# Performance work log

Hardware: AMD Instinct MI355X
Metric: run time of the kernel (lower is better)

The kernel has to match this reference:

```python
import jax, jax.numpy as jnp
import numpy as np

B = 32          # batch_size
S = 64          # num_subgraph
D = 8           # dim_multi_hot (module-level global in source repo)
NE = S * D      # num_edges = 512
NNODES = 1024
E = 150000      # incidence rows
IN_UNITS = [16, 32, 32]
OUT_UNITS = [32, 32, 16]


def _glorot(key, shape):
    # glorot_normal over last two dims (out, in)
    fan_out, fan_in = shape[-2], shape[-1]
    std = (2.0 / (fan_in + fan_out)) ** 0.5
    return std * jax.random.normal(key, shape, dtype=jnp.float32)


def setup_inputs() -> dict:
    key = jax.random.key(0)
    ks = jax.random.split(key, 10)
    nodes_features = jax.random.normal(ks[0], (NNODES * S, IN_UNITS[0]), dtype=jnp.float32)
    c0 = jax.random.randint(ks[1], (E,), 0, B, dtype=jnp.int32)
    c1 = jax.random.randint(ks[2], (E,), 0, NNODES, dtype=jnp.int32)
    c2 = jax.random.randint(ks[3], (E,), 0, S, dtype=jnp.int32)
    c3 = jax.random.randint(ks[4], (E,), 0, D, dtype=jnp.int32)
    incidence_matrix = jnp.stack([c0, c1, c2, c3], axis=1)
    return {
        'nodes_features': nodes_features,
        'in_core0': _glorot(ks[5], (NE, IN_UNITS[1], IN_UNITS[0])),
        'in_bias0': jnp.zeros((NE, IN_UNITS[1], 1), jnp.float32),
        'in_core1': _glorot(ks[6], (NE, IN_UNITS[2], IN_UNITS[1])),
        'in_bias1': jnp.zeros((NE, IN_UNITS[2], 1), jnp.float32),
        'out_core0': _glorot(ks[7], (NE, OUT_UNITS[1], OUT_UNITS[0])),
        'out_bias0': jnp.zeros((NE, OUT_UNITS[1], 1), jnp.float32),
        'out_core1': _glorot(ks[8], (NE, OUT_UNITS[2], OUT_UNITS[1])),
        'out_bias1': jnp.zeros((NE, OUT_UNITS[2], 1), jnp.float32),
        'incidence_matrix': incidence_matrix,
    }


def reference(nodes_features, in_core0, in_bias0, in_core1, in_bias1,
              out_core0, out_bias0, out_core1, out_bias1, incidence_matrix):
    c0 = incidence_matrix[:, 0]
    c1 = incidence_matrix[:, 1]
    c2 = incidence_matrix[:, 2]
    c3 = incidence_matrix[:, 3]

    # gather node features per incidence row: [E, in0]
    x = nodes_features[c1 * S + c2]
    eidx = c2 * D + c3  # per-edge weight index, < NE

    # per-edge MLP (gathered batched matmul + bias + relu)
    for W, b in ((in_core0, in_bias0), (in_core1, in_bias1)):
        x = jax.nn.relu(jnp.einsum('eoi,ei->eo', W[eidx], x) + b[eidx, :, 0])

    # unsorted segment mean over irregular edge groups
    seg = c0 * (D * S) + c2 * D + c3
    nseg = B * S * D
    sums = jax.ops.segment_sum(x, seg, num_segments=nseg)           # [B*NE, 32]
    cnt = jax.ops.segment_sum(jnp.ones((x.shape[0], 1), x.dtype), seg, num_segments=nseg)
    ef = jnp.where(cnt > 0, sums / jnp.maximum(cnt, 1.0), 0.0)       # [B*NE, 32]

    # output MLP: weights tiled over batch (einsum avoids explicit repeat)
    ef = ef.reshape(B, NE, -1)
    for W, b in ((out_core0, out_bias0), (out_core1, out_bias1)):
        ef = jax.nn.relu(jnp.einsum('eoi,bei->beo', W, ef) + b[None, :, :, 0])

    return ef.reshape(B * NE, OUT_UNITS[-1], 1)
```

## Files before the change

### kernel.cpp

```cpp
#include <hip/hip_runtime.h>

#define B_    32
#define S_    64
#define D_    8
#define NE_   512
#define E_    150000
#define CAP   448

#define SC_BLK   1024
#define SC_EPT   4
#define SC_EPB   (SC_BLK * SC_EPT)
#define SC_GRID  ((E_ + SC_EPB - 1) / SC_EPB)
#define SLOTS    32
#define PITCH    (SC_GRID * SLOTS)

#define PAYLOAD_BYTE_OFF 131072

typedef __attribute__((ext_vector_type(8)))  short  short8;
typedef __attribute__((ext_vector_type(16))) float  float16;

__device__ __forceinline__ unsigned short f2bf(float f) {
    union { float f; unsigned int u; } cv; cv.f = f;
    unsigned int u = cv.u;
    return (unsigned short)((u + 0x7fffu + ((u >> 16) & 1u)) >> 16);
}
__device__ __forceinline__ unsigned int pack2bf(float a, float b) {
    return (unsigned int)f2bf(a) | ((unsigned int)f2bf(b) << 16);
}

__global__ __launch_bounds__(SC_BLK)
void scatter_bin(const int* __restrict__ inc,
                 int* __restrict__ cnt2D,
                 int* __restrict__ payload2D) {
    __shared__ int lcount[NE_];
    const int tid = threadIdx.x;

    if (tid < NE_) lcount[tid] = 0;
    __syncthreads();

    int ei[SC_EPT], lp[SC_EPT], pl[SC_EPT];
    #pragma unroll
    for (int i = 0; i < SC_EPT; ++i) {
        const int e = blockIdx.x * SC_EPB + i * SC_BLK + tid;
        ei[i] = -1;
        if (e < E_) {
            const int4 c = ((const int4*)inc)[e];
            ei[i] = c.z * D_ + c.w;
            pl[i] = (c.x << 16) | (c.y * S_ + c.z);
            lp[i] = atomicAdd(&lcount[ei[i]], 1);
        }
    }
    #pragma unroll
    for (int i = 0; i < SC_EPT; ++i)
        if (ei[i] >= 0 && lp[i] < SLOTS)
            payload2D[ei[i] * PITCH + blockIdx.x * SLOTS + lp[i]] = pl[i];
    __syncthreads();
    if (tid < NE_)
        cnt2D[tid * SC_GRID + blockIdx.x] = min(lcount[tid], SLOTS);
}


#define TILE_COMPUTE(bXv, pvv, vldv)                                            \
  {                                                                             \
    float16 c0;                                                                 \
    _Pragma("unroll")                                                           \
    for (int r = 0; r < 16; ++r)                                                \
        c0[r] = bias0s[(r & 3) + 8 * (r >> 2) + 4 * q];                         \
    c0 = __builtin_amdgcn_mfma_f32_32x32x16_bf16(aWa, (bXv), c0, 0, 0, 0);      \
    unsigned Pw[8];                                                             \
    _Pragma("unroll")                                                           \
    for (int j = 0; j < 8; ++j)                                                 \
        Pw[j] = pack2bf(fmaxf(c0[2 * j], 0.f), fmaxf(c0[2 * j + 1], 0.f));      \
    asm("v_permlane32_swap_b32 %0, %1" : "+v"(Pw[0]), "+v"(Pw[2]));             \
    asm("v_permlane32_swap_b32 %0, %1" : "+v"(Pw[1]), "+v"(Pw[3]));             \
    asm("v_permlane32_swap_b32 %0, %1" : "+v"(Pw[4]), "+v"(Pw[6]));             \
    asm("v_permlane32_swap_b32 %0, %1" : "+v"(Pw[5]), "+v"(Pw[7]));             \
    union { unsigned u[4]; short8 s; } H0c, H1c;                                \
    H0c.u[0] = Pw[0]; H0c.u[1] = Pw[1]; H0c.u[2] = Pw[2]; H0c.u[3] = Pw[3];     \
    H1c.u[0] = Pw[4]; H1c.u[1] = Pw[5]; H1c.u[2] = Pw[6]; H1c.u[3] = Pw[7];     \
    float16 c1;                                                                 \
    _Pragma("unroll")                                                           \
    for (int r = 0; r < 16; ++r)                                                \
        c1[r] = bias1s[(r & 3) + 8 * (r >> 2) + 4 * q];                         \
    c1 = __builtin_amdgcn_mfma_f32_32x32x16_bf16(aWb0, H0c.s, c1, 0, 0, 0);     \
    c1 = __builtin_amdgcn_mfma_f32_32x32x16_bf16(aWb1, H1c.s, c1, 0, 0, 0);     \
    if (vldv) {                                                                 \
        const int b_e = ((pvv) >> 16) & 31;                                     \
        _Pragma("unroll")                                                       \
        for (int r = 0; r < 16; ++r)                                            \
            atomicAdd(&acc[b_e][(r & 3) + 8 * (r >> 2) + 4 * q],                \
                      fmaxf(c1[r], 0.f));                                       \
        if (q == 0) atomicAdd(&cnts[b_e], 1.f);                                 \
    }                                                                           \
  }

__global__ __launch_bounds__(512, 4)
void main_mfma(const float* __restrict__ nf,
               const float* __restrict__ iw0, const float* __restrict__ ib0,
               const float* __restrict__ iw1, const float* __restrict__ ib1,
               const float* __restrict__ ow0, const float* __restrict__ ob0,
               const float* __restrict__ ow1, const float* __restrict__ ob1,
               const int* __restrict__ cnt2D, const int* __restrict__ payload2D,
               float* __restrict__ out) {
    const int bid  = blockIdx.x;
    const int tid  = threadIdx.x;
    const int wav  = tid >> 6;
    const int lane = tid & 63;
    const int e32  = lane & 31;
    const int q    = lane >> 5;

    __shared__ float acc[32][33];
    __shared__ float hb[32][33];
    __shared__ float cnts[32];
    __shared__ float q0t[32 * 33];
    __shared__ float q1t[32 * 17];
    __shared__ float qb0s[32], qb1s[16];
    __shared__ float bias0s[32], bias1s[32];
    __shared__ int   sbase[64], scount[64];
    __shared__ int   sn;
    __shared__ int   elist[512];

    const int* Pb = payload2D + (size_t)bid * PITCH;
    const int p0 = tid, p1 = tid + 512, p2 = tid + 1024;
    const int r0 = Pb[p0];
    const int r1 = Pb[p1];
    const int r2 = (p2 < PITCH) ? Pb[p2] : 0;

    if (tid < 64) {
        int v = (tid < SC_GRID) ? cnt2D[bid * SC_GRID + tid] : 0;
        scount[tid] = v;
        int incl = v;
        #pragma unroll
        for (int off = 1; off < 64; off <<= 1) {
            const int t = __shfl_up(incl, off);
            if (tid >= off) incl += t;
        }
        sbase[tid] = incl - v;
        if (tid == SC_GRID - 1) sn = min(incl, CAP);
    }

    short8 aWa, aWb0, aWb1;
    {
        const float* wa = iw0 + (size_t)bid * 512 + e32 * 16 + q * 8;
        float4 u0 = ((const float4*)wa)[0], u1 = ((const float4*)wa)[1];
        unsigned int p[4] = { pack2bf(u0.x,u0.y), pack2bf(u0.z,u0.w),
                              pack2bf(u1.x,u1.y), pack2bf(u1.z,u1.w) };
        aWa = *(short8*)p;
    }
    {
        const float* wb = iw1 + (size_t)bid * 1024 + e32 * 32 + q * 8;
        float4 u0 = ((const float4*)wb)[0], u1 = ((const float4*)wb)[1];
        unsigned int p[4] = { pack2bf(u0.x,u0.y), pack2bf(u0.z,u0.w),
                              pack2bf(u1.x,u1.y), pack2bf(u1.z,u1.w) };
        aWb0 = *(short8*)p;
        const float* wb2 = wb + 16;
        float4 u2 = ((const float4*)wb2)[0], u3 = ((const float4*)wb2)[1];
        unsigned int p2k[4] = { pack2bf(u2.x,u2.y), pack2bf(u2.z,u2.w),
                                pack2bf(u3.x,u3.y), pack2bf(u3.z,u3.w) };
        aWb1 = *(short8*)p2k;
    }

    for (int i = tid; i < 1024; i += 512) {
        const int o = i >> 5, k = i & 31;
        q0t[k * 33 + o] = ow0[(size_t)bid * 1024 + i];
    }
    { const int o = tid >> 5, k = tid & 31;
      q1t[k * 17 + o] = ow1[(size_t)bid * 512 + tid]; }
    if (tid < 32)       { bias0s[tid] = ib0[bid * 32 + tid]; cnts[tid] = 0.f; }
    else if (tid < 64)  bias1s[tid - 32] = ib1[bid * 32 + (tid - 32)];
    else if (tid < 96)  qb0s[tid - 64] = ob0[bid * 32 + (tid - 64)];
    else if (tid < 112) qb1s[tid - 96] = ob1[bid * 16 + (tid - 96)];
    for (int i = tid; i < 32 * 33; i += 512) ((float*)acc)[i] = 0.f;
    __syncthreads();

    {
        const int blk0 = p0 >> 5, sl0 = p0 & 31;
        if (sl0 < scount[blk0]) {
            const int idx = sbase[blk0] + sl0;
            if (idx < CAP) elist[idx] = r0;
        }
        const int blk1 = p1 >> 5, sl1 = p1 & 31;
        if (sl1 < scount[blk1]) {
            const int idx = sbase[blk1] + sl1;
            if (idx < CAP) elist[idx] = r1;
        }
        if (p2 < PITCH) {
            const int blk2 = p2 >> 5, sl2 = p2 & 31;
            if (sl2 < scount[blk2]) {
                const int idx = sbase[blk2] + sl2;
                if (idx < CAP) elist[idx] = r2;
            }
        }
    }
    __syncthreads();

    const int n  = sn;
    const int s0 = (wav << 5) + e32;
    const int s1 = s0 + 256;
    const int pv0 = elist[s0];
    const int pv1 = elist[s1];
    const bool v0 = s0 < n;
    const bool v1 = s1 < n;

    short8 bX0, bX1;
    {
        const float4* xp = (const float4*)(nf + (size_t)(pv0 & 0xFFFF) * 16 + q * 8);
        float4 u0 = xp[0], u1 = xp[1];
        unsigned int pk[4] = { pack2bf(u0.x,u0.y), pack2bf(u0.z,u0.w),
                               pack2bf(u1.x,u1.y), pack2bf(u1.z,u1.w) };
        bX0 = *(short8*)pk;
    }
    {
        const float4* xp = (const float4*)(nf + (size_t)(pv1 & 0xFFFF) * 16 + q * 8);
        float4 u0 = xp[0], u1 = xp[1];
        unsigned int pk[4] = { pack2bf(u0.x,u0.y), pack2bf(u0.z,u0.w),
                               pack2bf(u1.x,u1.y), pack2bf(u1.z,u1.w) };
        bX1 = *(short8*)pk;
    }

    TILE_COMPUTE(bX0, pv0, v0);
    TILE_COMPUTE(bX1, pv1, v1);
    __syncthreads();

    {
        const int b  = tid >> 4;
        const int j  = tid & 15;
        const float cv  = cnts[b];
        const float inv = cv > 0.f ? 1.0f / cv : 0.0f;
        #pragma unroll
        for (int s = 0; s < 2; ++s) {
            const int oo = j * 2 + s;
            float d = 0.f;
            #pragma unroll
            for (int k = 0; k < 32; ++k) d = fmaf(q0t[k * 33 + oo], acc[b][k], d);
            hb[b][oo] = fmaxf(fmaf(d, inv, qb0s[oo]), 0.f);
        }
    }
    __syncthreads();

    {
        const int b = tid >> 4;
        const int o = tid & 15;
        float d = qb1s[o];
        #pragma unroll
        for (int k = 0; k < 32; ++k) d = fmaf(q1t[k * 17 + o], hb[b][k], d);
        out[((size_t)b * NE_ + bid) * 16 + o] = fmaxf(d, 0.f);
    }
}

extern "C" void kernel_launch(void* const* d_in, const int* in_sizes, int n_in,
                              void* d_out, int out_size, void* d_ws, size_t ws_size,
                              hipStream_t stream) {
    const float* nf  = (const float*)d_in[0];
    const float* iw0 = (const float*)d_in[1];
    const float* ib0 = (const float*)d_in[2];
    const float* iw1 = (const float*)d_in[3];
    const float* ib1 = (const float*)d_in[4];
    const float* ow0 = (const float*)d_in[5];
    const float* ob0 = (const float*)d_in[6];
    const float* ow1 = (const float*)d_in[7];
    const float* ob1 = (const float*)d_in[8];
    const int*   inc = (const int*)d_in[9];

    int* cnt2D     = (int*)d_ws;
    int* payload2D = (int*)((char*)d_ws + PAYLOAD_BYTE_OFF);

    scatter_bin<<<SC_GRID, SC_BLK, 0, stream>>>(inc, cnt2D, payload2D);
    main_mfma<<<NE_, 512, 0, stream>>>(nf, iw0, ib0, iw1, ib1, ow0, ob0, ow1, ob1,
                                       cnt2D, payload2D, (float*)d_out);
}
```

Before: 119.0 us.

## Gather node features before compaction and drop shared-memory scan barriers

Each wave now does the per-block prefix scan itself with shuffles, so the shared scount/sbase arrays and one __syncthreads are gone. Node-feature rows are gathered and packed to bf16 right after the payload load. They are stored into LDS next to the compacted edge list, which removes the dependent global gather after compaction and overlaps it with the weight loads. The two output-MLP stages are merged without a barrier between them, which relies on each batch row's hb being produced within the same wavefront. The trade-off is gathering for every payload slot, including unused ones, plus 16 KB more LDS per block, which may reduce occupancy.

```diff
diff --git a/kernel.cpp b/kernel.cpp
--- a/kernel.cpp
+++ b/kernel.cpp
@@ -94,6 +94,16 @@
     }                                                                           \
   }
 
+#define GATHER_PACK(rowv, LO, HI)                                               \
+  {                                                                             \
+    const float4* xp = (const float4*)(nf + (size_t)(rowv) * 16);               \
+    float4 a0 = xp[0], a1 = xp[1], a2 = xp[2], a3 = xp[3];                      \
+    LO.x = pack2bf(a0.x, a0.y); LO.y = pack2bf(a0.z, a0.w);                     \
+    LO.z = pack2bf(a1.x, a1.y); LO.w = pack2bf(a1.z, a1.w);                     \
+    HI.x = pack2bf(a2.x, a2.y); HI.y = pack2bf(a2.z, a2.w);                     \
+    HI.z = pack2bf(a3.x, a3.y); HI.w = pack2bf(a3.z, a3.w);                     \
+  }
+
 __global__ __launch_bounds__(512, 4)
 void main_mfma(const float* __restrict__ nf,
                const float* __restrict__ iw0, const float* __restrict__ ib0,
@@ -109,6 +119,9 @@
     const int e32  = lane & 31;
     const int q    = lane >> 5;
 
+    __shared__ uint4 xls0[512];
+    __shared__ uint4 xls1[512];
+    __shared__ int   elist[512];
     __shared__ float acc[32][33];
     __shared__ float hb[32][33];
     __shared__ float cnts[32];
@@ -116,28 +129,25 @@
     __shared__ float q1t[32 * 17];
     __shared__ float qb0s[32], qb1s[16];
     __shared__ float bias0s[32], bias1s[32];
-    __shared__ int   sbase[64], scount[64];
-    __shared__ int   sn;
-    __shared__ int   elist[512];
+
 
     const int* Pb = payload2D + (size_t)bid * PITCH;
     const int p0 = tid, p1 = tid + 512, p2 = tid + 1024;
     const int r0 = Pb[p0];
     const int r1 = Pb[p1];
-    const int r2 = (p2 < PITCH) ? Pb[p2] : 0;
-
-    if (tid < 64) {
-        int v = (tid < SC_GRID) ? cnt2D[bid * SC_GRID + tid] : 0;
-        scount[tid] = v;
-        int incl = v;
-        #pragma unroll
-        for (int off = 1; off < 64; off <<= 1) {
-            const int t = __shfl_up(incl, off);
-            if (tid >= off) incl += t;
-        }
-        sbase[tid] = incl - v;
-        if (tid == SC_GRID - 1) sn = min(incl, CAP);
-    }
+    int r2 = 0;
+    if (p2 < PITCH) r2 = Pb[p2];
+
+    int v = 0;
+    if (lane < SC_GRID) v = cnt2D[bid * SC_GRID + lane];
+    int incl = v;
+    #pragma unroll
+    for (int off = 1; off < 64; off <<= 1) {
+        const int t = __shfl_up(incl, off);
+        if (lane >= off) incl += t;
+    }
+    const int excl = incl - v;
+    const int n = min(__shfl(incl, SC_GRID - 1), CAP);
 
     short8 aWa, aWb0, aWb1;
     {
@@ -160,6 +170,11 @@
         aWb1 = *(short8*)p2k;
     }
 
+    uint4 g0lo = {}, g0hi = {}, g1lo = {}, g1hi = {}, g2lo = {}, g2hi = {};
+    GATHER_PACK(r0 & 0xFFFF, g0lo, g0hi);
+    GATHER_PACK(r1 & 0xFFFF, g1lo, g1hi);
+    GATHER_PACK(r2 & 0xFFFF, g2lo, g2hi);
+
     for (int i = tid; i < 1024; i += 512) {
         const int o = i >> 5, k = i & 31;
         q0t[k * 33 + o] = ow0[(size_t)bid * 1024 + i];
@@ -171,52 +186,37 @@
     else if (tid < 96)  qb0s[tid - 64] = ob0[bid * 32 + (tid - 64)];
     else if (tid < 112) qb1s[tid - 96] = ob1[bid * 16 + (tid - 96)];
     for (int i = tid; i < 32 * 33; i += 512) ((float*)acc)[i] = 0.f;
-    __syncthreads();
-
-    {
-        const int blk0 = p0 >> 5, sl0 = p0 & 31;
-        if (sl0 < scount[blk0]) {
-            const int idx = sbase[blk0] + sl0;
-            if (idx < CAP) elist[idx] = r0;
-        }
-        const int blk1 = p1 >> 5, sl1 = p1 & 31;
-        if (sl1 < scount[blk1]) {
-            const int idx = sbase[blk1] + sl1;
-            if (idx < CAP) elist[idx] = r1;
-        }
-        if (p2 < PITCH) {
-            const int blk2 = p2 >> 5, sl2 = p2 & 31;
-            if (sl2 < scount[blk2]) {
-                const int idx = sbase[blk2] + sl2;
-                if (idx < CAP) elist[idx] = r2;
-            }
-        }
-    }
-    __syncthreads();
-
-    const int n  = sn;
+
+    {
+        const int blk0 = p0 >> 5,                 sl0 = p0 & 31;
+        const int blk1 = p1 >> 5,                 sl1 = p1 & 31;
+        const int blk2 = min(p2 >> 5, SC_GRID-1), sl2 = p2 & 31;
+        const int c0_ = __shfl(v, blk0),   b0_ = __shfl(excl, blk0);
+        const int c1_ = __shfl(v, blk1),   b1_ = __shfl(excl, blk1);
+        const int c2_ = __shfl(v, blk2),   b2_ = __shfl(excl, blk2);
+        if (sl0 < c0_) {
+            const int idx = b0_ + sl0;
+            if (idx < CAP) { elist[idx] = r0; xls0[idx] = g0lo; xls1[idx] = g0hi; }
+        }
+        if (sl1 < c1_) {
+            const int idx = b1_ + sl1;
+            if (idx < CAP) { elist[idx] = r1; xls0[idx] = g1lo; xls1[idx] = g1hi; }
+        }
+        if (p2 < PITCH && sl2 < c2_) {
+            const int idx = b2_ + sl2;
+            if (idx < CAP) { elist[idx] = r2; xls0[idx] = g2lo; xls1[idx] = g2hi; }
+        }
+    }
+    __syncthreads();
+
     const int s0 = (wav << 5) + e32;
     const int s1 = s0 + 256;
     const int pv0 = elist[s0];
     const int pv1 = elist[s1];
     const bool v0 = s0 < n;
     const bool v1 = s1 < n;
-
-    short8 bX0, bX1;
-    {
-        const float4* xp = (const float4*)(nf + (size_t)(pv0 & 0xFFFF) * 16 + q * 8);
-        float4 u0 = xp[0], u1 = xp[1];
-        unsigned int pk[4] = { pack2bf(u0.x,u0.y), pack2bf(u0.z,u0.w),
-                               pack2bf(u1.x,u1.y), pack2bf(u1.z,u1.w) };
-        bX0 = *(short8*)pk;
-    }
-    {
-        const float4* xp = (const float4*)(nf + (size_t)(pv1 & 0xFFFF) * 16 + q * 8);
-        float4 u0 = xp[0], u1 = xp[1];
-        unsigned int pk[4] = { pack2bf(u0.x,u0.y), pack2bf(u0.z,u0.w),
-                               pack2bf(u1.x,u1.y), pack2bf(u1.z,u1.w) };
-        bX1 = *(short8*)pk;
-    }
+    const short8 bX0 = *(const short8*)(q ? &xls1[s0] : &xls0[s0]);
+    const short8 bX1 = *(const short8*)(q ? &xls1[s1] : &xls0[s1]);
 
     TILE_COMPUTE(bX0, pv0, v0);
     TILE_COMPUTE(bX1, pv1, v1);
@@ -235,16 +235,10 @@
             for (int k = 0; k < 32; ++k) d = fmaf(q0t[k * 33 + oo], acc[b][k], d);
             hb[b][oo] = fmaxf(fmaf(d, inv, qb0s[oo]), 0.f);
         }
-    }
-    __syncthreads();
-
-    {
-        const int b = tid >> 4;
-        const int o = tid & 15;
-        float d = qb1s[o];
+        float d1 = qb1s[j];
         #pragma unroll
-        for (int k = 0; k < 32; ++k) d = fmaf(q1t[k * 17 + o], hb[b][k], d);
-        out[((size_t)b * NE_ + bid) * 16 + o] = fmaxf(d, 0.f);
+        for (int k = 0; k < 32; ++k) d1 = fmaf(q1t[k * 17 + j], hb[b][k], d1);
+        out[((size_t)b * NE_ + bid) * 16 + j] = fmaxf(d1, 0.f);
     }
 }
 
```

New measurement: 119.5 us. Within noise of the previous version (+0.3%).
